# Kernel tuning notes

Measured on AMD Instinct MI355X. Metric: run time of the kernel, lower is better.

The kernel has to match this reference:

```python
import jax, jax.numpy as jnp
import numpy as np
from jax import lax

DIM = 1024
HID = 2048          # dim * hidden_mult(2)
E = 8               # num_experts
K = 2               # top_k
B, T = 2, 512


def setup_inputs() -> dict:
    key = jax.random.key(0)
    ks = jax.random.split(key, 5)
    scale = 1.0 / np.sqrt(DIM)
    x = jax.random.normal(ks[0], (B, T, DIM), dtype=jnp.float32)
    router_w = jax.random.normal(ks[1], (E, DIM), dtype=jnp.float32) * scale   # Linear(dim, E) weight (out,in)
    w_gate = jax.random.normal(ks[2], (E, HID, DIM), dtype=jnp.float32) * scale
    w_up = jax.random.normal(ks[3], (E, HID, DIM), dtype=jnp.float32) * scale
    w_down = jax.random.normal(ks[4], (E, DIM, HID), dtype=jnp.float32) * (1.0 / np.sqrt(HID))
    return {"x": x, "router_w": router_w, "w_gate": w_gate, "w_up": w_up, "w_down": w_down}


def reference(x, router_w, w_gate, w_up, w_down):
    Bb, Tt, D = x.shape
    N = Bb * Tt
    xf = x.reshape(N, D)
    # router + top-k gating (weights renormalized over selected experts)
    logits = xf @ router_w.T                                   # (N, E)
    routing = jax.nn.softmax(logits, axis=-1)
    top_w, top_i = lax.top_k(routing, K)                       # (N, K)
    top_w = top_w / jnp.sum(top_w, axis=-1, keepdims=True)
    # combine weights: per-token weight for each expert (0 if not selected).
    # Multiplying by 0 reproduces the mask-gather-scatter loop exactly.
    combine = jnp.zeros((N, E), dtype=x.dtype)
    combine = combine.at[jnp.arange(N)[:, None], top_i].add(top_w)  # (N, E)
    # SwiGLU experts, batched over the (small, fixed) expert axis
    g = jnp.einsum('nd,ehd->neh', xf, w_gate)                  # (N, E, H)
    u = jnp.einsum('nd,ehd->neh', xf, w_up)
    h = jax.nn.silu(g) * u
    y = jnp.einsum('neh,edh->ned', h, w_down)                  # (N, E, D)
    out = jnp.einsum('ned,ne->nd', y, combine)
    return out.reshape(Bb, Tt, D)
```

## Files before the change

kernel.cpp:

```cpp
#include <hip/hip_runtime.h>
#include <hip/hip_bf16.h>
#include <math.h>

#define DIM 1024
#define HID 2048
#define NEXP 8
#define NTOK 1024
#define TOPK 2

typedef __attribute__((ext_vector_type(4))) float f32x4;
typedef __attribute__((ext_vector_type(8))) short bf16x8;
typedef __attribute__((ext_vector_type(4))) short bf16x4;

__device__ inline bf16x4 cvt4(f32x4 v) {
    bf16x4 r;
#pragma unroll
    for (int i = 0; i < 4; ++i) {
        union { float f; unsigned u; } t; t.f = v[i];
        unsigned b = t.u + 0x7fffu + ((t.u >> 16) & 1u);
        r[i] = (short)(b >> 16);
    }
    return r;
}

__global__ __launch_bounds__(256) void xcvt_kernel(const float* __restrict__ x, __hip_bfloat16* __restrict__ xb)
{
    int i = blockIdx.x * 256 + threadIdx.x;
    f32x4 v = *(const f32x4*)(x + (size_t)i * 4);
    *(bf16x4*)(xb + (size_t)i * 4) = cvt4(v);
}

__global__ __launch_bounds__(64) void router_kernel(
    const float* __restrict__ x, const float* __restrict__ rw,
    int* __restrict__ counts, int* __restrict__ slot_list, float* __restrict__ w_list)
{
    int t = blockIdx.x;
    int lane = threadIdx.x;
    const float* xr = x + (size_t)t * DIM;
    float acc[NEXP];
#pragma unroll
    for (int e = 0; e < NEXP; ++e) acc[e] = 0.f;
    for (int d = lane; d < DIM; d += 64) {
        float xv = xr[d];
#pragma unroll
        for (int e = 0; e < NEXP; ++e) acc[e] += xv * rw[e * DIM + d];
    }
#pragma unroll
    for (int off = 32; off > 0; off >>= 1) {
#pragma unroll
        for (int e = 0; e < NEXP; ++e) acc[e] += __shfl_down(acc[e], off, 64);
    }
    if (lane == 0) {
        int i1 = 0;
#pragma unroll
        for (int e = 1; e < NEXP; ++e) if (acc[e] > acc[i1]) i1 = e;
        int i2 = -1;
#pragma unroll
        for (int e = 0; e < NEXP; ++e) {
            if (e == i1) continue;
            if (i2 < 0 || acc[e] > acc[i2]) i2 = e;
        }
        float w1 = 1.f / (1.f + expf(acc[i2] - acc[i1]));
        float w2 = 1.f - w1;
        int p1 = atomicAdd(&counts[i1], 1);
        slot_list[i1 * NTOK + p1] = t * 2 + 0;
        w_list[i1 * NTOK + p1] = w1;
        int p2 = atomicAdd(&counts[i2], 1);
        slot_list[i2 * NTOK + p2] = t * 2 + 1;
        w_list[i2 * NTOK + p2] = w2;
    }
}

#define LDK 72
#define MBLK 128

__global__ __launch_bounds__(256, 2) void gateup_mfma(
    const __hip_bfloat16* __restrict__ xb, const float* __restrict__ wg, const float* __restrict__ wu,
    const int* __restrict__ counts, const int* __restrict__ slot_list, const float* __restrict__ w_list,
    __hip_bfloat16* __restrict__ h_buf)
{
    __shared__ short Xs[2][MBLK * LDK];
    __shared__ short Gs[2][64 * LDK];
    __shared__ short Us[2][64 * LDK];

    int bid = blockIdx.x;
    int pl = bid & 7, s = bid >> 3;
    int z = s & 1, ph = s >> 1;
    int p = (ph << 3) + pl;
    int e = p >> 5;
    int hbase = (p & 31) * 64;

    int n_e = counts[e];
    const float* WG = wg + (size_t)e * HID * DIM;
    const float* WU = wu + (size_t)e * HID * DIM;
    const int* sl = slot_list + e * NTOK;
    const float* wl = w_list + e * NTOK;

    int tid = threadIdx.x;
    int lane = tid & 63;
    int wn = tid >> 6;
    int fr = lane & 15, fq = lane >> 4;

    int c8 = tid & 7;
    int xrr = tid >> 3;
    int c4 = tid & 15;
    int wrr = tid >> 4;

    for (int m0 = z * MBLK; m0 < n_e; m0 += 2 * MBLK) {
        int rows = n_e - m0; if (rows > MBLK) rows = MBLK;

        const __hip_bfloat16* xsrc[4];
#pragma unroll
        for (int p_ = 0; p_ < 4; ++p_) {
            int r = p_ * 32 + xrr;
            xsrc[p_] = (r < rows) ? (xb + (size_t)(sl[m0 + r] >> 1) * DIM + c8 * 8) : (const __hip_bfloat16*)0;
        }
        const float* gsrc[4]; const float* usrc[4];
#pragma unroll
        for (int p_ = 0; p_ < 4; ++p_) {
            int r = p_ * 16 + wrr;
            gsrc[p_] = WG + (size_t)(hbase + r) * DIM + c4 * 4;
            usrc[p_] = WU + (size_t)(hbase + r) * DIM + c4 * 4;
        }

        bf16x8 xr[4]; f32x4 gr[4], ur[4];
#pragma unroll
        for (int p_ = 0; p_ < 4; ++p_) {
            bf16x8 xv = (bf16x8)(short)0;
            if (xsrc[p_]) xv = *(const bf16x8*)(xsrc[p_]);
            xr[p_] = xv;
            gr[p_] = *(const f32x4*)(gsrc[p_]);
            ur[p_] = *(const f32x4*)(usrc[p_]);
        }

        f32x4 accg[8], accu[8];
#pragma unroll
        for (int ms = 0; ms < 8; ++ms) { accg[ms] = (f32x4)(0.f); accu[ms] = (f32x4)(0.f); }

#pragma unroll 1
        for (int t = 0; t < DIM / 64; ++t) {
            int cur = t & 1;
#pragma unroll
            for (int p_ = 0; p_ < 4; ++p_)
                *(bf16x8*)&Xs[cur][(p_ * 32 + xrr) * LDK + c8 * 8] = xr[p_];
#pragma unroll
            for (int p_ = 0; p_ < 4; ++p_) {
                *(bf16x4*)&Gs[cur][(p_ * 16 + wrr) * LDK + c4 * 4] = cvt4(gr[p_]);
                *(bf16x4*)&Us[cur][(p_ * 16 + wrr) * LDK + c4 * 4] = cvt4(ur[p_]);
            }
            __syncthreads();
            if (t + 1 < DIM / 64) {
                int ko = (t + 1) * 64;
#pragma unroll
                for (int p_ = 0; p_ < 4; ++p_) {
                    bf16x8 xv = (bf16x8)(short)0;
                    if (xsrc[p_]) xv = *(const bf16x8*)(xsrc[p_] + ko);
                    xr[p_] = xv;
                    gr[p_] = *(const f32x4*)(gsrc[p_] + ko);
                    ur[p_] = *(const f32x4*)(usrc[p_] + ko);
                }
            }
#pragma unroll
            for (int kk = 0; kk < 2; ++kk) {
                int kof = kk * 32 + fq * 8;
                bf16x8 bg = *(const bf16x8*)&Gs[cur][(wn * 16 + fr) * LDK + kof];
                bf16x8 bu = *(const bf16x8*)&Us[cur][(wn * 16 + fr) * LDK + kof];
#pragma unroll
                for (int ms = 0; ms < 8; ++ms) {
                    bf16x8 a = *(const bf16x8*)&Xs[cur][(ms * 16 + fr) * LDK + kof];
                    accg[ms] = __builtin_amdgcn_mfma_f32_16x16x32_bf16(a, bg, accg[ms], 0, 0, 0);
                    accu[ms] = __builtin_amdgcn_mfma_f32_16x16x32_bf16(a, bu, accu[ms], 0, 0, 0);
                }
            }
            __syncthreads();
        }

#pragma unroll
        for (int ms = 0; ms < 8; ++ms) {
#pragma unroll
            for (int reg = 0; reg < 4; ++reg) {
                int r = ms * 16 + fq * 4 + reg;
                if (r < rows) {
                    int slot = sl[m0 + r];
                    float w = wl[m0 + r];
                    float g = accg[ms][reg], u = accu[ms][reg];
                    float h = w * (g / (1.f + expf(-g))) * u;
                    h_buf[(size_t)slot * HID + hbase + wn * 16 + fr] = __float2bfloat16(h);
                }
            }
        }
    }
}

__global__ __launch_bounds__(256, 2) void down_mfma(
    const __hip_bfloat16* __restrict__ h_buf, const float* __restrict__ wd,
    const int* __restrict__ counts, const int* __restrict__ slot_list,
    float* __restrict__ ybuf)
{
    __shared__ short Hs[2][MBLK * LDK];
    __shared__ short Ws[2][64 * LDK];

    int bid = blockIdx.x;
    int pl = bid & 7, s = bid >> 3;
    int z = s & 1, ph = s >> 1;
    int q = (ph << 3) + pl;
    int e = q >> 4;
    int dbase = (q & 15) * 64;

    int n_e = counts[e];
    const float* WD = wd + (size_t)e * DIM * HID;
    const int* sl = slot_list + e * NTOK;

    int tid = threadIdx.x;
    int lane = tid & 63;
    int wn = tid >> 6;
    int fr = lane & 15, fq = lane >> 4;

    int c8 = tid & 7;
    int hrr = tid >> 3;
    int c4 = tid & 15;
    int wrr = tid >> 4;

    for (int m0 = z * MBLK; m0 < n_e; m0 += 2 * MBLK) {
        int rows = n_e - m0; if (rows > MBLK) rows = MBLK;

        const __hip_bfloat16* hsrc[4];
#pragma unroll
        for (int p_ = 0; p_ < 4; ++p_) {
            int r = p_ * 32 + hrr;
            hsrc[p_] = (r < rows) ? (h_buf + (size_t)sl[m0 + r] * HID + c8 * 8) : (const __hip_bfloat16*)0;
        }
        const float* wsrc[4];
#pragma unroll
        for (int p_ = 0; p_ < 4; ++p_)
            wsrc[p_] = WD + (size_t)(dbase + p_ * 16 + wrr) * HID + c4 * 4;

        bf16x8 hr_[4]; f32x4 wr_[4];
#pragma unroll
        for (int p_ = 0; p_ < 4; ++p_) {
            bf16x8 hv = (bf16x8)(short)0;
            if (hsrc[p_]) hv = *(const bf16x8*)(hsrc[p_]);
            hr_[p_] = hv;
            wr_[p_] = *(const f32x4*)(wsrc[p_]);
        }

        f32x4 acc[8];
#pragma unroll
        for (int ms = 0; ms < 8; ++ms) acc[ms] = (f32x4)(0.f);

#pragma unroll 1
        for (int t = 0; t < HID / 64; ++t) {
            int cur = t & 1;
#pragma unroll
            for (int p_ = 0; p_ < 4; ++p_)
                *(bf16x8*)&Hs[cur][(p_ * 32 + hrr) * LDK + c8 * 8] = hr_[p_];
#pragma unroll
            for (int p_ = 0; p_ < 4; ++p_)
                *(bf16x4*)&Ws[cur][(p_ * 16 + wrr) * LDK + c4 * 4] = cvt4(wr_[p_]);
            __syncthreads();
            if (t + 1 < HID / 64) {
                int ko = (t + 1) * 64;
#pragma unroll
                for (int p_ = 0; p_ < 4; ++p_) {
                    bf16x8 hv = (bf16x8)(short)0;
                    if (hsrc[p_]) hv = *(const bf16x8*)(hsrc[p_] + ko);
                    hr_[p_] = hv;
                    wr_[p_] = *(const f32x4*)(wsrc[p_] + ko);
                }
            }
#pragma unroll
            for (int kk = 0; kk < 2; ++kk) {
                int kof = kk * 32 + fq * 8;
                bf16x8 b = *(const bf16x8*)&Ws[cur][(wn * 16 + fr) * LDK + kof];
#pragma unroll
                for (int ms = 0; ms < 8; ++ms) {
                    bf16x8 a = *(const bf16x8*)&Hs[cur][(ms * 16 + fr) * LDK + kof];
                    acc[ms] = __builtin_amdgcn_mfma_f32_16x16x32_bf16(a, b, acc[ms], 0, 0, 0);
                }
            }
            __syncthreads();
        }

#pragma unroll
        for (int ms = 0; ms < 8; ++ms) {
#pragma unroll
            for (int reg = 0; reg < 4; ++reg) {
                int r = ms * 16 + fq * 4 + reg;
                if (r < rows) {
                    int slot = sl[m0 + r];
                    ybuf[(size_t)slot * DIM + dbase + wn * 16 + fr] = acc[ms][reg];
                }
            }
        }
    }
}

__global__ __launch_bounds__(256) void combine_kernel(const float* __restrict__ ybuf, float* __restrict__ out)
{
    int i = blockIdx.x * 256 + threadIdx.x;
    int t = i >> 8;
    int c = i & 255;
    const float4* ya = (const float4*)(ybuf + (size_t)(2 * t) * DIM) + c;
    const float4* yb = (const float4*)(ybuf + (size_t)(2 * t + 1) * DIM) + c;
    float4 a = *ya, b = *yb, r;
    r.x = a.x + b.x; r.y = a.y + b.y; r.z = a.z + b.z; r.w = a.w + b.w;
    ((float4*)(out + (size_t)t * DIM))[c] = r;
}

extern "C" void kernel_launch(void* const* d_in, const int* in_sizes, int n_in,
                              void* d_out, int out_size, void* d_ws, size_t ws_size,
                              hipStream_t stream) {
    const float* x  = (const float*)d_in[0];
    const float* rw = (const float*)d_in[1];
    const float* wg = (const float*)d_in[2];
    const float* wu = (const float*)d_in[3];
    const float* wd = (const float*)d_in[4];
    float* out = (float*)d_out;

    char* ws = (char*)d_ws;
    int* counts            = (int*)ws;
    int* slot_list         = (int*)(ws + 256);
    float* w_list          = (float*)(ws + 256 + NEXP * NTOK * 4);
    __hip_bfloat16* xb     = (__hip_bfloat16*)(ws + 256 + 2 * NEXP * NTOK * 4);
    __hip_bfloat16* h_buf  = (__hip_bfloat16*)((char*)xb + (size_t)NTOK * DIM * 2);
    float* ybuf            = (float*)((char*)h_buf + (size_t)NTOK * TOPK * HID * 2);

    hipMemsetAsync(counts, 0, NEXP * sizeof(int), stream);
    xcvt_kernel<<<NTOK * DIM / 4 / 256, 256, 0, stream>>>(x, xb);
    router_kernel<<<NTOK, 64, 0, stream>>>(x, rw, counts, slot_list, w_list);
    gateup_mfma<<<512, 256, 0, stream>>>(xb, wg, wu, counts, slot_list, w_list, h_buf);
    down_mfma<<<256, 256, 0, stream>>>(h_buf, wd, counts, slot_list, ybuf);
    combine_kernel<<<NTOK * DIM / 4 / 256, 256, 0, stream>>>(ybuf, out);
}
```

Baseline: 164.9 us.

## Load MFMA operands directly from global memory, drop LDS staging and barriers

```diff
diff --git a/kernel.cpp b/kernel.cpp
--- a/kernel.cpp
+++ b/kernel.cpp
@@ -12,14 +12,20 @@
 typedef __attribute__((ext_vector_type(8))) short bf16x8;
 typedef __attribute__((ext_vector_type(4))) short bf16x4;
 
+__device__ inline short bf1(float f) {
+    __hip_bfloat16 b = __float2bfloat16(f);
+    union { __hip_bfloat16 b; short s; } u; u.b = b; return u.s;
+}
 __device__ inline bf16x4 cvt4(f32x4 v) {
     bf16x4 r;
 #pragma unroll
-    for (int i = 0; i < 4; ++i) {
-        union { float f; unsigned u; } t; t.f = v[i];
-        unsigned b = t.u + 0x7fffu + ((t.u >> 16) & 1u);
-        r[i] = (short)(b >> 16);
-    }
+    for (int i = 0; i < 4; ++i) r[i] = bf1(v[i]);
+    return r;
+}
+__device__ inline bf16x8 cat8(bf16x4 lo, bf16x4 hi) {
+    bf16x8 r;
+#pragma unroll
+    for (int i = 0; i < 4; ++i) { r[i] = lo[i]; r[i + 4] = hi[i]; }
     return r;
 }
 
@@ -71,18 +77,11 @@
     }
 }
 
-#define LDK 72
-#define MBLK 128
-
-__global__ __launch_bounds__(256, 2) void gateup_mfma(
+__global__ __launch_bounds__(256) void gateup_mfma(
     const __hip_bfloat16* __restrict__ xb, const float* __restrict__ wg, const float* __restrict__ wu,
     const int* __restrict__ counts, const int* __restrict__ slot_list, const float* __restrict__ w_list,
-    __hip_bfloat16* __restrict__ h_buf)
-{
-    __shared__ short Xs[2][MBLK * LDK];
-    __shared__ short Gs[2][64 * LDK];
-    __shared__ short Us[2][64 * LDK];
-
+    const __hip_bfloat16* __restrict__ zrow, __hip_bfloat16* __restrict__ h_buf)
+{
     int bid = blockIdx.x;
     int pl = bid & 7, s = bid >> 3;
     int z = s & 1, ph = s >> 1;
@@ -91,8 +90,7 @@
     int hbase = (p & 31) * 64;
 
     int n_e = counts[e];
-    const float* WG = wg + (size_t)e * HID * DIM;
-    const float* WU = wu + (size_t)e * HID * DIM;
+    if (n_e == 0) return;
     const int* sl = slot_list + e * NTOK;
     const float* wl = w_list + e * NTOK;
 
@@ -101,78 +99,56 @@
     int wn = tid >> 6;
     int fr = lane & 15, fq = lane >> 4;
 
-    int c8 = tid & 7;
-    int xrr = tid >> 3;
-    int c4 = tid & 15;
-    int wrr = tid >> 4;
-
-    for (int m0 = z * MBLK; m0 < n_e; m0 += 2 * MBLK) {
-        int rows = n_e - m0; if (rows > MBLK) rows = MBLK;
-
-        const __hip_bfloat16* xsrc[4];
-#pragma unroll
-        for (int p_ = 0; p_ < 4; ++p_) {
-            int r = p_ * 32 + xrr;
-            xsrc[p_] = (r < rows) ? (xb + (size_t)(sl[m0 + r] >> 1) * DIM + c8 * 8) : (const __hip_bfloat16*)0;
-        }
-        const float* gsrc[4]; const float* usrc[4];
-#pragma unroll
-        for (int p_ = 0; p_ < 4; ++p_) {
-            int r = p_ * 16 + wrr;
-            gsrc[p_] = WG + (size_t)(hbase + r) * DIM + c4 * 4;
-            usrc[p_] = WU + (size_t)(hbase + r) * DIM + c4 * 4;
-        }
-
-        bf16x8 xr[4]; f32x4 gr[4], ur[4];
-#pragma unroll
-        for (int p_ = 0; p_ < 4; ++p_) {
-            bf16x8 xv = (bf16x8)(short)0;
-            if (xsrc[p_]) xv = *(const bf16x8*)(xsrc[p_]);
-            xr[p_] = xv;
-            gr[p_] = *(const f32x4*)(gsrc[p_]);
-            ur[p_] = *(const f32x4*)(usrc[p_]);
+    const float* gp = wg + (size_t)e * HID * DIM + (size_t)(hbase + wn * 16 + fr) * DIM + fq * 8;
+    const float* up = wu + (size_t)e * HID * DIM + (size_t)(hbase + wn * 16 + fr) * DIM + fq * 8;
+
+    for (int m0 = z * 128; m0 < n_e; m0 += 256) {
+        int rows = n_e - m0; if (rows > 128) rows = 128;
+
+        const __hip_bfloat16* ap[8];
+#pragma unroll
+        for (int ms = 0; ms < 8; ++ms) {
+            int r = ms * 16 + fr;
+            ap[ms] = (r < rows) ? (xb + (size_t)(sl[m0 + r] >> 1) * DIM + fq * 8) : (zrow + fq * 8);
         }
 
         f32x4 accg[8], accu[8];
 #pragma unroll
         for (int ms = 0; ms < 8; ++ms) { accg[ms] = (f32x4)(0.f); accu[ms] = (f32x4)(0.f); }
+
+        f32x4 gpre[4], upre[4];
+#pragma unroll
+        for (int q2 = 0; q2 < 4; ++q2) {
+            gpre[q2] = *(const f32x4*)(gp + (q2 >> 1) * 32 + (q2 & 1) * 4);
+            upre[q2] = *(const f32x4*)(up + (q2 >> 1) * 32 + (q2 & 1) * 4);
+        }
 
 #pragma unroll 1
         for (int t = 0; t < DIM / 64; ++t) {
-            int cur = t & 1;
-#pragma unroll
-            for (int p_ = 0; p_ < 4; ++p_)
-                *(bf16x8*)&Xs[cur][(p_ * 32 + xrr) * LDK + c8 * 8] = xr[p_];
-#pragma unroll
-            for (int p_ = 0; p_ < 4; ++p_) {
-                *(bf16x4*)&Gs[cur][(p_ * 16 + wrr) * LDK + c4 * 4] = cvt4(gr[p_]);
-                *(bf16x4*)&Us[cur][(p_ * 16 + wrr) * LDK + c4 * 4] = cvt4(ur[p_]);
-            }
-            __syncthreads();
+            bf16x8 bg[2], bu[2];
+#pragma unroll
+            for (int kk = 0; kk < 2; ++kk) {
+                bg[kk] = cat8(cvt4(gpre[2 * kk]), cvt4(gpre[2 * kk + 1]));
+                bu[kk] = cat8(cvt4(upre[2 * kk]), cvt4(upre[2 * kk + 1]));
+            }
             if (t + 1 < DIM / 64) {
                 int ko = (t + 1) * 64;
 #pragma unroll
-                for (int p_ = 0; p_ < 4; ++p_) {
-                    bf16x8 xv = (bf16x8)(short)0;
-                    if (xsrc[p_]) xv = *(const bf16x8*)(xsrc[p_] + ko);
-                    xr[p_] = xv;
-                    gr[p_] = *(const f32x4*)(gsrc[p_] + ko);
-                    ur[p_] = *(const f32x4*)(usrc[p_] + ko);
+                for (int q2 = 0; q2 < 4; ++q2) {
+                    gpre[q2] = *(const f32x4*)(gp + ko + (q2 >> 1) * 32 + (q2 & 1) * 4);
+                    upre[q2] = *(const f32x4*)(up + ko + (q2 >> 1) * 32 + (q2 & 1) * 4);
                 }
             }
 #pragma unroll
             for (int kk = 0; kk < 2; ++kk) {
-                int kof = kk * 32 + fq * 8;
-                bf16x8 bg = *(const bf16x8*)&Gs[cur][(wn * 16 + fr) * LDK + kof];
-                bf16x8 bu = *(const bf16x8*)&Us[cur][(wn * 16 + fr) * LDK + kof];
+                int ao = t * 64 + kk * 32;
 #pragma unroll
                 for (int ms = 0; ms < 8; ++ms) {
-                    bf16x8 a = *(const bf16x8*)&Xs[cur][(ms * 16 + fr) * LDK + kof];
-                    accg[ms] = __builtin_amdgcn_mfma_f32_16x16x32_bf16(a, bg, accg[ms], 0, 0, 0);
-                    accu[ms] = __builtin_amdgcn_mfma_f32_16x16x32_bf16(a, bu, accu[ms], 0, 0, 0);
-                }
-            }
-            __syncthreads();
+                    bf16x8 a = *(const bf16x8*)(ap[ms] + ao);
+                    accg[ms] = __builtin_amdgcn_mfma_f32_16x16x32_bf16(a, bg[kk], accg[ms], 0, 0, 0);
+                    accu[ms] = __builtin_amdgcn_mfma_f32_16x16x32_bf16(a, bu[kk], accu[ms], 0, 0, 0);
+                }
+            }
         }
 
 #pragma unroll
@@ -192,23 +168,20 @@
     }
 }
 
-__global__ __launch_bounds__(256, 2) void down_mfma(
+__global__ __launch_bounds__(256) void down_mfma(
     const __hip_bfloat16* __restrict__ h_buf, const float* __restrict__ wd,
     const int* __restrict__ counts, const int* __restrict__ slot_list,
-    float* __restrict__ ybuf)
-{
-    __shared__ short Hs[2][MBLK * LDK];
-    __shared__ short Ws[2][64 * LDK];
-
+    const __hip_bfloat16* __restrict__ zrow, float* __restrict__ ybuf)
+{
     int bid = blockIdx.x;
     int pl = bid & 7, s = bid >> 3;
-    int z = s & 1, ph = s >> 1;
-    int q = (ph << 3) + pl;
+    int z = s & 3, qh = s >> 2;
+    int q = (qh << 3) + pl;
     int e = q >> 4;
     int dbase = (q & 15) * 64;
 
     int n_e = counts[e];
-    const float* WD = wd + (size_t)e * DIM * HID;
+    if (n_e == 0) return;
     const int* sl = slot_list + e * NTOK;
 
     int tid = threadIdx.x;
@@ -216,73 +189,52 @@
     int wn = tid >> 6;
     int fr = lane & 15, fq = lane >> 4;
 
-    int c8 = tid & 7;
-    int hrr = tid >> 3;
-    int c4 = tid & 15;
-    int wrr = tid >> 4;
-
-    for (int m0 = z * MBLK; m0 < n_e; m0 += 2 * MBLK) {
-        int rows = n_e - m0; if (rows > MBLK) rows = MBLK;
-
-        const __hip_bfloat16* hsrc[4];
-#pragma unroll
-        for (int p_ = 0; p_ < 4; ++p_) {
-            int r = p_ * 32 + hrr;
-            hsrc[p_] = (r < rows) ? (h_buf + (size_t)sl[m0 + r] * HID + c8 * 8) : (const __hip_bfloat16*)0;
-        }
-        const float* wsrc[4];
-#pragma unroll
-        for (int p_ = 0; p_ < 4; ++p_)
-            wsrc[p_] = WD + (size_t)(dbase + p_ * 16 + wrr) * HID + c4 * 4;
-
-        bf16x8 hr_[4]; f32x4 wr_[4];
-#pragma unroll
-        for (int p_ = 0; p_ < 4; ++p_) {
-            bf16x8 hv = (bf16x8)(short)0;
-            if (hsrc[p_]) hv = *(const bf16x8*)(hsrc[p_]);
-            hr_[p_] = hv;
-            wr_[p_] = *(const f32x4*)(wsrc[p_]);
-        }
-
-        f32x4 acc[8];
-#pragma unroll
-        for (int ms = 0; ms < 8; ++ms) acc[ms] = (f32x4)(0.f);
+    const float* wp = wd + (size_t)e * DIM * HID + (size_t)(dbase + wn * 16 + fr) * HID + fq * 8;
+
+    for (int m0 = z * 64; m0 < n_e; m0 += 256) {
+        int rows = n_e - m0; if (rows > 64) rows = 64;
+
+        const __hip_bfloat16* ap[4];
+#pragma unroll
+        for (int ms = 0; ms < 4; ++ms) {
+            int r = ms * 16 + fr;
+            ap[ms] = (r < rows) ? (h_buf + (size_t)sl[m0 + r] * HID + fq * 8) : (zrow + fq * 8);
+        }
+
+        f32x4 acc[4];
+#pragma unroll
+        for (int ms = 0; ms < 4; ++ms) acc[ms] = (f32x4)(0.f);
+
+        f32x4 wpre[4];
+#pragma unroll
+        for (int q2 = 0; q2 < 4; ++q2)
+            wpre[q2] = *(const f32x4*)(wp + (q2 >> 1) * 32 + (q2 & 1) * 4);
 
 #pragma unroll 1
         for (int t = 0; t < HID / 64; ++t) {
-            int cur = t & 1;
-#pragma unroll
-            for (int p_ = 0; p_ < 4; ++p_)
-                *(bf16x8*)&Hs[cur][(p_ * 32 + hrr) * LDK + c8 * 8] = hr_[p_];
-#pragma unroll
-            for (int p_ = 0; p_ < 4; ++p_)
-                *(bf16x4*)&Ws[cur][(p_ * 16 + wrr) * LDK + c4 * 4] = cvt4(wr_[p_]);
-            __syncthreads();
+            bf16x8 b[2];
+#pragma unroll
+            for (int kk = 0; kk < 2; ++kk)
+                b[kk] = cat8(cvt4(wpre[2 * kk]), cvt4(wpre[2 * kk + 1]));
             if (t + 1 < HID / 64) {
                 int ko = (t + 1) * 64;
 #pragma unroll
-                for (int p_ = 0; p_ < 4; ++p_) {
-                    bf16x8 hv = (bf16x8)(short)0;
-                    if (hsrc[p_]) hv = *(const bf16x8*)(hsrc[p_] + ko);
-                    hr_[p_] = hv;
-                    wr_[p_] = *(const f32x4*)(wsrc[p_] + ko);
-                }
+                for (int q2 = 0; q2 < 4; ++q2)
+                    wpre[q2] = *(const f32x4*)(wp + ko + (q2 >> 1) * 32 + (q2 & 1) * 4);
             }
 #pragma unroll
             for (int kk = 0; kk < 2; ++kk) {
-                int kof = kk * 32 + fq * 8;
-                bf16x8 b = *(const bf16x8*)&Ws[cur][(wn * 16 + fr) * LDK + kof];
-#pragma unroll
-                for (int ms = 0; ms < 8; ++ms) {
-                    bf16x8 a = *(const bf16x8*)&Hs[cur][(ms * 16 + fr) * LDK + kof];
-                    acc[ms] = __builtin_amdgcn_mfma_f32_16x16x32_bf16(a, b, acc[ms], 0, 0, 0);
-                }
-            }
-            __syncthreads();
-        }
-
-#pragma unroll
-        for (int ms = 0; ms < 8; ++ms) {
+                int ao = t * 64 + kk * 32;
+#pragma unroll
+                for (int ms = 0; ms < 4; ++ms) {
+                    bf16x8 a = *(const bf16x8*)(ap[ms] + ao);
+                    acc[ms] = __builtin_amdgcn_mfma_f32_16x16x32_bf16(a, b[kk], acc[ms], 0, 0, 0);
+                }
+            }
+        }
+
+#pragma unroll
+        for (int ms = 0; ms < 4; ++ms) {
 #pragma unroll
             for (int reg = 0; reg < 4; ++reg) {
                 int r = ms * 16 + fq * 4 + reg;
@@ -324,11 +276,13 @@
     __hip_bfloat16* xb     = (__hip_bfloat16*)(ws + 256 + 2 * NEXP * NTOK * 4);
     __hip_bfloat16* h_buf  = (__hip_bfloat16*)((char*)xb + (size_t)NTOK * DIM * 2);
     float* ybuf            = (float*)((char*)h_buf + (size_t)NTOK * TOPK * HID * 2);
+    __hip_bfloat16* zrow   = (__hip_bfloat16*)((char*)ybuf + (size_t)NTOK * TOPK * DIM * 4);
 
     hipMemsetAsync(counts, 0, NEXP * sizeof(int), stream);
+    hipMemsetAsync(zrow, 0, HID * sizeof(__hip_bfloat16), stream);
     xcvt_kernel<<<NTOK * DIM / 4 / 256, 256, 0, stream>>>(x, xb);
     router_kernel<<<NTOK, 64, 0, stream>>>(x, rw, counts, slot_list, w_list);
-    gateup_mfma<<<512, 256, 0, stream>>>(xb, wg, wu, counts, slot_list, w_list, h_buf);
-    down_mfma<<<256, 256, 0, stream>>>(h_buf, wd, counts, slot_list, ybuf);
+    gateup_mfma<<<512, 256, 0, stream>>>(xb, wg, wu, counts, slot_list, w_list, zrow, h_buf);
+    down_mfma<<<512, 256, 0, stream>>>(h_buf, wd, counts, slot_list, zrow, ybuf);
     combine_kernel<<<NTOK * DIM / 4 / 256, 256, 0, stream>>>(ybuf, out);
 }
```

Measured after the change: 362.3 us. +119.7%, slower.
